# Optimization experiments

Hardware: AMD Instinct MI355X
Metric: run time of the kernel (lower is better)

## Reference

```python
import jax, jax.numpy as jnp
import numpy as np
from math import pi

TWO_PI = 2.0 * pi

def ringify(x):
    return (x + pi) % TWO_PI - pi

def complex_mean(x, axes):
    dir_x = ringify(jnp.cos(x)).sum(axis=axes)
    dir_y = jnp.sin(x).sum(axis=axes)
    return jnp.arctan2(dir_y, dir_x)

def extract_patches(x, k, s):
    # x: (B, C, H, W) -> (B, Ho, Wo, C, k, k)
    B, C, H, W = x.shape
    Ho = (H - k) // s + 1
    Wo = (W - k) // s + 1
    idx_h = jnp.arange(Ho)[:, None] * s + jnp.arange(k)[None, :]  # (Ho, k)
    idx_w = jnp.arange(Wo)[:, None] * s + jnp.arange(k)[None, :]  # (Wo, k)
    # advanced indexing on dims 2,3 with broadcast shape (Ho, Wo, k, k)
    p = x[:, :, idx_h[:, None, :, None], idx_w[None, :, None, :]]  # (B, C, Ho, Wo, k, k)
    return p.transpose(0, 2, 3, 1, 4, 5)

def ring_conv2d(x, weight, kernel_size, stride):
    # x: (B, C, H, W); weight: (O, C, k, k) -> out: (B, Ho, Wo, O)
    patches = extract_patches(x, kernel_size, stride)            # (B,Ho,Wo,C,k,k)
    w = weight.transpose(1, 2, 3, 0)                              # (C,k,k,O)
    diff = ringify(patches[..., None] - w)                        # (B,Ho,Wo,C,k,k,O)
    return complex_mean(diff, axes=(-4, -3, -2))                  # (B,Ho,Wo,O)

def setup_inputs() -> dict:
    key = jax.random.key(0)
    k1, k2, k3, k4 = jax.random.split(key, 4)
    return {
        "x": jax.random.normal(k1, (4096, 1, 28, 28), dtype=jnp.float32),
        "conv1_weight": jax.random.normal(k2, (4, 1, 2, 2), dtype=jnp.float32),
        "conv2_weight": jax.random.normal(k3, (8, 4, 4, 4), dtype=jnp.float32),
        "ff_weight": jax.random.normal(k4, (288, 10), dtype=jnp.float32),
    }

def reference(x, conv1_weight, conv2_weight, ff_weight):
    h = ringify(x).reshape(-1, 1, 28, 28)
    h = ring_conv2d(h, conv1_weight, kernel_size=2, stride=2)     # (B,14,14,4)
    h = h.transpose(0, 3, 1, 2)                                   # (B,4,14,14)
    h = ring_conv2d(h, conv2_weight, kernel_size=4, stride=2)     # (B,6,6,8)
    h = h.reshape(h.shape[0], -1)                                 # (B,288)
    h = complex_mean(ringify(h[:, :, None] - ff_weight), axes=(-2,))  # (B,10)
    return jnp.sin(h)
```

## Files before the change

### kernel.cpp

```cpp
#include <hip/hip_runtime.h>

#define WT_W1 0
#define WT_W2 16
#define WT_FF 528

typedef _Float16 h2 __attribute__((ext_vector_type(2)));

__device__ __forceinline__ float fdot2(unsigned a, unsigned b, float c) {
    return __builtin_amdgcn_fdot2(__builtin_bit_cast(h2, a),
                                  __builtin_bit_cast(h2, b), c, false);
}
__device__ __forceinline__ unsigned packh2(float x, float y) {
    h2 h; h.x = (_Float16)x; h.y = (_Float16)y;
    return __builtin_bit_cast(unsigned, h);
}

__global__ void ringnn_setup(const float* __restrict__ w1,
                             const float* __restrict__ w2,
                             const float* __restrict__ ffw,
                             uint2* __restrict__ wt) {
    int t = blockIdx.x * blockDim.x + threadIdx.x;
    if (t >= 3408) return;
    float a;
    if (t < 16)        a = w1[t];
    else if (t < 528)  a = w2[t - 16];
    else               a = ffw[t - 528];
    float s, c;
    __sincosf(a, &s, &c);
    uint2 v;
    v.x = packh2(c, s);
    v.y = packh2(-s, c);
    wt[t] = v;
}

__global__ __launch_bounds__(256) void ringnn_main(
    const float* __restrict__ x,
    const uint2* __restrict__ wt,
    float* __restrict__ out)
{
    __shared__ unsigned cs1[2][784];
    __shared__ unsigned cs2[2][288];

    const int t    = threadIdx.x;
    const int img  = t >> 7;
    const int tid  = t & 127;
    const int b    = blockIdx.x * 2 + img;
    const float* xb = x + b * 784;

    for (int pos = tid; pos < 196; pos += 128) {
        const int i = pos / 14;
        const int j = pos - i * 14;
        const float* px = xb + (2 * i) * 28 + 2 * j;
        float2 p0 = *(const float2*)(px);
        float2 p1 = *(const float2*)(px + 28);
        float s0, c0, s1, c1, s2, c2, s3, c3;
        __sincosf(p0.x, &s0, &c0);
        __sincosf(p0.y, &s1, &c1);
        __sincosf(p1.x, &s2, &c2);
        __sincosf(p1.y, &s3, &c3);
        unsigned v0 = packh2(c0, s0), v1 = packh2(c1, s1);
        unsigned v2 = packh2(c2, s2), v3 = packh2(c3, s3);
        #pragma unroll
        for (int o = 0; o < 4; ++o) {
            uint2 wa = wt[WT_W1 + o * 4 + 0], wb = wt[WT_W1 + o * 4 + 1];
            uint2 wc = wt[WT_W1 + o * 4 + 2], wd = wt[WT_W1 + o * 4 + 3];
            float X = 0.f, Y = 0.f;
            X = fdot2(v0, wa.x, X); Y = fdot2(v0, wa.y, Y);
            X = fdot2(v1, wb.x, X); Y = fdot2(v1, wb.y, Y);
            X = fdot2(v2, wc.x, X); Y = fdot2(v2, wc.y, Y);
            X = fdot2(v3, wd.x, X); Y = fdot2(v3, wd.y, Y);
            float rinv = rsqrtf(fmaxf(fmaf(X, X, Y * Y), 1e-30f));
            cs1[img][o * 196 + pos] = packh2(X * rinv, Y * rinv);
        }
    }
    __syncthreads();

    {
        const int wave  = t >> 6;
        const int lane  = t & 63;
        const int img2  = wave >> 1;
        const int ohalf = __builtin_amdgcn_readfirstlane(wave & 1);
        if (lane < 36) {
            const int i = lane / 6;
            const int j = lane - i * 6;
            const unsigned* cb = &cs1[img2][(2 * i) * 14 + 2 * j];
            float X[4] = {0.f, 0.f, 0.f, 0.f};
            float Y[4] = {0.f, 0.f, 0.f, 0.f};
            #pragma unroll
            for (int c = 0; c < 4; ++c) {
                uint2 a[4][2];
                #pragma unroll
                for (int dy = 0; dy < 4; ++dy) {
                    const unsigned* r = cb + c * 196 + dy * 14;
                    a[dy][0] = *(const uint2*)(r);
                    a[dy][1] = *(const uint2*)(r + 2);
                }
                #pragma unroll
                for (int oo = 0; oo < 4; ++oo) {
                    const uint2* wp = wt + WT_W2 + (ohalf * 4 + oo) * 64 + c * 16;
                    #pragma unroll
                    for (int dy = 0; dy < 4; ++dy) {
                        uint2 w0 = wp[dy * 4 + 0], w1_ = wp[dy * 4 + 1];
                        uint2 w2_ = wp[dy * 4 + 2], w3 = wp[dy * 4 + 3];
                        unsigned va = a[dy][0].x, vb = a[dy][0].y;
                        unsigned vc = a[dy][1].x, vd = a[dy][1].y;
                        X[oo] = fdot2(va, w0.x, X[oo]); Y[oo] = fdot2(va, w0.y, Y[oo]);
                        X[oo] = fdot2(vb, w1_.x, X[oo]); Y[oo] = fdot2(vb, w1_.y, Y[oo]);
                        X[oo] = fdot2(vc, w2_.x, X[oo]); Y[oo] = fdot2(vc, w2_.y, Y[oo]);
                        X[oo] = fdot2(vd, w3.x, X[oo]); Y[oo] = fdot2(vd, w3.y, Y[oo]);
                    }
                }
            }
            unsigned r0, r1, r2, r3;
            {
                float rv0 = rsqrtf(fmaxf(fmaf(X[0], X[0], Y[0] * Y[0]), 1e-30f));
                float rv1 = rsqrtf(fmaxf(fmaf(X[1], X[1], Y[1] * Y[1]), 1e-30f));
                float rv2 = rsqrtf(fmaxf(fmaf(X[2], X[2], Y[2] * Y[2]), 1e-30f));
                float rv3 = rsqrtf(fmaxf(fmaf(X[3], X[3], Y[3] * Y[3]), 1e-30f));
                r0 = packh2(X[0] * rv0, Y[0] * rv0);
                r1 = packh2(X[1] * rv1, Y[1] * rv1);
                r2 = packh2(X[2] * rv2, Y[2] * rv2);
                r3 = packh2(X[3] * rv3, Y[3] * rv3);
            }
            uint2* dst = (uint2*)&cs2[img2][lane * 8 + ohalf * 4];
            dst[0] = make_uint2(r0, r1);
            dst[1] = make_uint2(r2, r3);
        }
    }
    __syncthreads();

    float2* red = (float2*)cs1[img];
    {
        float X = 0.f, Y = 0.f;
        const int n = tid / 12;
        const int g = tid - n * 12;
        if (n < 10) {
            #pragma unroll 6
            for (int k = 0; k < 24; ++k) {
                const int f = g + 12 * k;
                unsigned v = cs2[img][f];
                uint2 wvv = wt[WT_FF + f * 10 + n];
                X = fdot2(v, wvv.x, X);
                Y = fdot2(v, wvv.y, Y);
            }
        }
        red[tid] = make_float2(X, Y);
    }
    __syncthreads();
    if (tid < 10) {
        float Xs = 0.f, Ys = 0.f;
        #pragma unroll
        for (int g2 = 0; g2 < 12; ++g2) {
            float2 p = red[tid * 12 + g2];
            Xs += p.x; Ys += p.y;
        }
        float rinv = rsqrtf(fmaxf(fmaf(Xs, Xs, Ys * Ys), 1e-30f));
        out[b * 10 + tid] = Ys * rinv;
    }
}

extern "C" void kernel_launch(void* const* d_in, const int* in_sizes, int n_in,
                              void* d_out, int out_size, void* d_ws, size_t ws_size,
                              hipStream_t stream) {
    const float* x   = (const float*)d_in[0];
    const float* w1  = (const float*)d_in[1];
    const float* w2  = (const float*)d_in[2];
    const float* ffw = (const float*)d_in[3];
    uint2* wt = (uint2*)d_ws;
    float* o  = (float*)d_out;

    ringnn_setup<<<14, 256, 0, stream>>>(w1, w2, ffw, wt);
    ringnn_main<<<2048, 256, 0, stream>>>(x, wt, o);
}
```

Measured before the change: 82.22 us.

## Assign one image per wavefront and drop block-level barriers

Each 64-lane wave now processes one whole image through all three stages, so every __syncthreads is removed and only intra-wave LDS ordering is relied on. Conv2 computes all 8 output channels per lane instead of splitting them across two waves. The final reduction uses lane shuffles instead of an LDS scratch pass. In exchange, conv1 and the FF stage use fewer threads per image, conv2 holds more accumulators per lane, and 28 lanes sit idle during conv2.

```diff
diff --git a/kernel.cpp b/kernel.cpp
--- a/kernel.cpp
+++ b/kernel.cpp
@@ -38,16 +38,16 @@
     const uint2* __restrict__ wt,
     float* __restrict__ out)
 {
-    __shared__ unsigned cs1[2][784];
-    __shared__ unsigned cs2[2][288];
+    __shared__ unsigned cs1[4][784];
+    __shared__ unsigned cs2[4][288];
 
     const int t    = threadIdx.x;
-    const int img  = t >> 7;
-    const int tid  = t & 127;
-    const int b    = blockIdx.x * 2 + img;
+    const int wv   = t >> 6;
+    const int lane = t & 63;
+    const int b    = blockIdx.x * 4 + wv;
     const float* xb = x + b * 784;
 
-    for (int pos = tid; pos < 196; pos += 128) {
+    for (int pos = lane; pos < 196; pos += 64) {
         const int i = pos / 14;
         const int j = pos - i * 14;
         const float* px = xb + (2 * i) * 28 + 2 * j;
@@ -70,92 +70,89 @@
             X = fdot2(v2, wc.x, X); Y = fdot2(v2, wc.y, Y);
             X = fdot2(v3, wd.x, X); Y = fdot2(v3, wd.y, Y);
             float rinv = rsqrtf(fmaxf(fmaf(X, X, Y * Y), 1e-30f));
-            cs1[img][o * 196 + pos] = packh2(X * rinv, Y * rinv);
+            cs1[wv][o * 196 + pos] = packh2(X * rinv, Y * rinv);
         }
     }
-    __syncthreads();
+
+    if (lane < 36) {
+        const int i = lane / 6;
+        const int j = lane - i * 6;
+        const unsigned* cb = &cs1[wv][(2 * i) * 14 + 2 * j];
+        float X0=0.f,X1=0.f,X2=0.f,X3=0.f,X4=0.f,X5=0.f,X6=0.f,X7=0.f;
+        float Y0=0.f,Y1=0.f,Y2=0.f,Y3=0.f,Y4=0.f,Y5=0.f,Y6=0.f,Y7=0.f;
+        #pragma unroll
+        for (int c = 0; c < 4; ++c) {
+            uint2 a[4][2];
+            #pragma unroll
+            for (int dy = 0; dy < 4; ++dy) {
+                const unsigned* r = cb + c * 196 + dy * 14;
+                a[dy][0] = *(const uint2*)(r);
+                a[dy][1] = *(const uint2*)(r + 2);
+            }
+            #pragma unroll
+            for (int o = 0; o < 8; ++o) {
+                float Xa = 0.f, Ya = 0.f;
+                const uint2* wp = wt + WT_W2 + o * 64 + c * 16;
+                #pragma unroll
+                for (int dy = 0; dy < 4; ++dy) {
+                    uint2 w0 = wp[dy * 4 + 0], w1_ = wp[dy * 4 + 1];
+                    uint2 w2_ = wp[dy * 4 + 2], w3_ = wp[dy * 4 + 3];
+                    Xa = fdot2(a[dy][0].x, w0.x, Xa); Ya = fdot2(a[dy][0].x, w0.y, Ya);
+                    Xa = fdot2(a[dy][0].y, w1_.x, Xa); Ya = fdot2(a[dy][0].y, w1_.y, Ya);
+                    Xa = fdot2(a[dy][1].x, w2_.x, Xa); Ya = fdot2(a[dy][1].x, w2_.y, Ya);
+                    Xa = fdot2(a[dy][1].y, w3_.x, Xa); Ya = fdot2(a[dy][1].y, w3_.y, Ya);
+                }
+                switch (o) {
+                    case 0: X0 += Xa; Y0 += Ya; break;
+                    case 1: X1 += Xa; Y1 += Ya; break;
+                    case 2: X2 += Xa; Y2 += Ya; break;
+                    case 3: X3 += Xa; Y3 += Ya; break;
+                    case 4: X4 += Xa; Y4 += Ya; break;
+                    case 5: X5 += Xa; Y5 += Ya; break;
+                    case 6: X6 += Xa; Y6 += Ya; break;
+                    case 7: X7 += Xa; Y7 += Ya; break;
+                }
+            }
+        }
+        unsigned rr[8];
+        {
+            float Xs[8] = {X0,X1,X2,X3,X4,X5,X6,X7};
+            float Ys[8] = {Y0,Y1,Y2,Y3,Y4,Y5,Y6,Y7};
+            #pragma unroll
+            for (int o = 0; o < 8; ++o) {
+                float rv = rsqrtf(fmaxf(fmaf(Xs[o], Xs[o], Ys[o] * Ys[o]), 1e-30f));
+                rr[o] = packh2(Xs[o] * rv, Ys[o] * rv);
+            }
+        }
+        uint2* dst = (uint2*)&cs2[wv][lane * 8];
+        dst[0] = make_uint2(rr[0], rr[1]);
+        dst[1] = make_uint2(rr[2], rr[3]);
+        dst[2] = make_uint2(rr[4], rr[5]);
+        dst[3] = make_uint2(rr[6], rr[7]);
+    }
 
     {
-        const int wave  = t >> 6;
-        const int lane  = t & 63;
-        const int img2  = wave >> 1;
-        const int ohalf = __builtin_amdgcn_readfirstlane(wave & 1);
-        if (lane < 36) {
-            const int i = lane / 6;
-            const int j = lane - i * 6;
-            const unsigned* cb = &cs1[img2][(2 * i) * 14 + 2 * j];
-            float X[4] = {0.f, 0.f, 0.f, 0.f};
-            float Y[4] = {0.f, 0.f, 0.f, 0.f};
-            #pragma unroll
-            for (int c = 0; c < 4; ++c) {
-                uint2 a[4][2];
-                #pragma unroll
-                for (int dy = 0; dy < 4; ++dy) {
-                    const unsigned* r = cb + c * 196 + dy * 14;
-                    a[dy][0] = *(const uint2*)(r);
-                    a[dy][1] = *(const uint2*)(r + 2);
-                }
-                #pragma unroll
-                for (int oo = 0; oo < 4; ++oo) {
-                    const uint2* wp = wt + WT_W2 + (ohalf * 4 + oo) * 64 + c * 16;
-                    #pragma unroll
-                    for (int dy = 0; dy < 4; ++dy) {
-                        uint2 w0 = wp[dy * 4 + 0], w1_ = wp[dy * 4 + 1];
-                        uint2 w2_ = wp[dy * 4 + 2], w3 = wp[dy * 4 + 3];
-                        unsigned va = a[dy][0].x, vb = a[dy][0].y;
-                        unsigned vc = a[dy][1].x, vd = a[dy][1].y;
-                        X[oo] = fdot2(va, w0.x, X[oo]); Y[oo] = fdot2(va, w0.y, Y[oo]);
-                        X[oo] = fdot2(vb, w1_.x, X[oo]); Y[oo] = fdot2(vb, w1_.y, Y[oo]);
-                        X[oo] = fdot2(vc, w2_.x, X[oo]); Y[oo] = fdot2(vc, w2_.y, Y[oo]);
-                        X[oo] = fdot2(vd, w3.x, X[oo]); Y[oo] = fdot2(vd, w3.y, Y[oo]);
-                    }
-                }
-            }
-            unsigned r0, r1, r2, r3;
-            {
-                float rv0 = rsqrtf(fmaxf(fmaf(X[0], X[0], Y[0] * Y[0]), 1e-30f));
-                float rv1 = rsqrtf(fmaxf(fmaf(X[1], X[1], Y[1] * Y[1]), 1e-30f));
-                float rv2 = rsqrtf(fmaxf(fmaf(X[2], X[2], Y[2] * Y[2]), 1e-30f));
-                float rv3 = rsqrtf(fmaxf(fmaf(X[3], X[3], Y[3] * Y[3]), 1e-30f));
-                r0 = packh2(X[0] * rv0, Y[0] * rv0);
-                r1 = packh2(X[1] * rv1, Y[1] * rv1);
-                r2 = packh2(X[2] * rv2, Y[2] * rv2);
-                r3 = packh2(X[3] * rv3, Y[3] * rv3);
-            }
-            uint2* dst = (uint2*)&cs2[img2][lane * 8 + ohalf * 4];
-            dst[0] = make_uint2(r0, r1);
-            dst[1] = make_uint2(r2, r3);
-        }
-    }
-    __syncthreads();
-
-    float2* red = (float2*)cs1[img];
-    {
         float X = 0.f, Y = 0.f;
-        const int n = tid / 12;
-        const int g = tid - n * 12;
+        const int n = lane / 6;
+        const int g = lane - n * 6;
         if (n < 10) {
             #pragma unroll 6
-            for (int k = 0; k < 24; ++k) {
-                const int f = g + 12 * k;
-                unsigned v = cs2[img][f];
+            for (int k = 0; k < 48; ++k) {
+                const int f = g + 6 * k;
+                unsigned v = cs2[wv][f];
                 uint2 wvv = wt[WT_FF + f * 10 + n];
                 X = fdot2(v, wvv.x, X);
                 Y = fdot2(v, wvv.y, Y);
             }
         }
-        red[tid] = make_float2(X, Y);
-    }
-    __syncthreads();
-    if (tid < 10) {
-        float Xs = 0.f, Ys = 0.f;
-        #pragma unroll
-        for (int g2 = 0; g2 < 12; ++g2) {
-            float2 p = red[tid * 12 + g2];
-            Xs += p.x; Ys += p.y;
+        float pX = X + __shfl_down(X, 3);
+        float pY = Y + __shfl_down(Y, 3);
+        float sX = pX + __shfl_down(pX, 1) + __shfl_down(pX, 2);
+        float sY = pY + __shfl_down(pY, 1) + __shfl_down(pY, 2);
+        if (g == 0 && n < 10) {
+            float rinv = rsqrtf(fmaxf(fmaf(sX, sX, sY * sY), 1e-30f));
+            out[b * 10 + n] = sY * rinv;
         }
-        float rinv = rsqrtf(fmaxf(fmaf(Xs, Xs, Ys * Ys), 1e-30f));
-        out[b * 10 + tid] = Ys * rinv;
     }
 }
 
@@ -170,5 +167,5 @@
     float* o  = (float*)d_out;
 
     ringnn_setup<<<14, 256, 0, stream>>>(w1, w2, ffw, wt);
-    ringnn_main<<<2048, 256, 0, stream>>>(x, wt, o);
+    ringnn_main<<<1024, 256, 0, stream>>>(x, wt, o);
 }
```

Measured after the change: 85.82 us. 1.04x slower.
